# Performance work log

Hardware: AMD Instinct MI355X
Metric: run time of the kernel (lower is better)

Reference implementation:

```python
import jax, jax.numpy as jnp
import numpy as np
import math

NUM_HEADS = 16
D_KV = 64
D_MODEL = 1024
NUM_BUCKETS = 32
MAX_DISTANCE = 128
SEQ = 2048
BATCH = 2


def _relative_position_bucket(relative_position):
    # bidirectional T5 bucketing
    num_buckets = NUM_BUCKETS // 2  # 16
    buckets = (relative_position > 0).astype(jnp.int32) * num_buckets
    rp = jnp.abs(relative_position)
    max_exact = num_buckets // 2  # 8
    is_small = rp < max_exact
    rp_safe = jnp.maximum(rp, 1)  # avoid log(0); masked by is_small anyway
    rp_large = max_exact + (
        jnp.log(rp_safe.astype(jnp.float32) / max_exact)
        / math.log(MAX_DISTANCE / max_exact)
        * (num_buckets - max_exact)
    ).astype(jnp.int32)
    rp_large = jnp.minimum(rp_large, num_buckets - 1)
    return buckets + jnp.where(is_small, rp, rp_large)


def _position_bias(rel_bias_table, q_len, k_len):
    ctx = jnp.arange(q_len)[:, None]
    mem = jnp.arange(k_len)[None, :]
    buckets = _relative_position_bucket(mem - ctx)  # (q,k)
    vals = rel_bias_table[buckets]  # (q,k,h)
    return jnp.transpose(vals, (2, 0, 1))[None]  # (1,h,q,k)


def setup_inputs() -> dict:
    key = jax.random.key(0)
    ks = jax.random.split(key, 6)
    s = 1.0 / math.sqrt(D_MODEL)
    return {
        "hidden_states": jax.random.normal(ks[0], (BATCH, SEQ, D_MODEL), jnp.float32),
        "Wq": jax.random.normal(ks[1], (D_MODEL, NUM_HEADS * D_KV), jnp.float32) * s,
        "Wk": jax.random.normal(ks[2], (D_MODEL, NUM_HEADS * D_KV), jnp.float32) * s,
        "Wv": jax.random.normal(ks[3], (D_MODEL, NUM_HEADS * D_KV), jnp.float32) * s,
        "Wo": jax.random.normal(ks[4], (NUM_HEADS * D_KV, D_MODEL), jnp.float32) * s,
        "rel_bias_table": jax.random.normal(ks[5], (NUM_BUCKETS, NUM_HEADS), jnp.float32),
    }


def reference(hidden_states, Wq, Wk, Wv, Wo, rel_bias_table):
    b, s, _ = hidden_states.shape
    q = (hidden_states @ Wq).reshape(b, s, NUM_HEADS, D_KV).transpose(0, 2, 1, 3)
    k = (hidden_states @ Wk).reshape(b, s, NUM_HEADS, D_KV).transpose(0, 2, 1, 3)
    v = (hidden_states @ Wv).reshape(b, s, NUM_HEADS, D_KV).transpose(0, 2, 1, 3)
    # T5: NO query scaling, additive relative-position bias
    scores = jnp.einsum("bhqd,bhkd->bhqk", q, k) + _position_bias(rel_bias_table, s, s)
    attn = jax.nn.softmax(scores, axis=-1)  # dropout is identity in eval
    out = jnp.einsum("bhqk,bhkd->bhqd", attn, v)
    out = out.transpose(0, 2, 1, 3).reshape(b, s, NUM_HEADS * D_KV)
    return out @ Wo
```

## Files before the change

### kernel.cpp

```cpp
#include <hip/hip_runtime.h>
#include <hip/hip_bf16.h>
#include <math.h>

#define NUM_HEADS 16
#define D_KV 64
#define D_MODEL 1024
#define SEQ 2048
#define BATCH 2
#define LOG2E 1.4426950408889634f

using bf16x8 = __attribute__((ext_vector_type(8))) short;
using bf16x4 = __attribute__((ext_vector_type(4))) short;
using f32x4  = __attribute__((ext_vector_type(4))) float;

__device__ inline unsigned short f2bf(float f) {
  union { float f; unsigned int i; } v; v.f = f;
  unsigned int u = v.i;
  return (unsigned short)((u + 0x7FFFu + ((u >> 16) & 1u)) >> 16);
}
__device__ inline unsigned short f2bf_fast(float f) {
  union { float f; unsigned int i; } v; v.f = f;
  return (unsigned short)((v.i + 0x8000u) >> 16);
}

#if __has_builtin(__builtin_amdgcn_exp2f)
#define EXP2(x) __builtin_amdgcn_exp2f(x)
#else
#define EXP2(x) __expf((x) * 0.6931471805599453f)
#endif

__device__ inline unsigned int pk_bf16(float a, float b) {
#if __has_builtin(__builtin_amdgcn_cvt_pk_bf16_f32)
  auto v = __builtin_amdgcn_cvt_pk_bf16_f32(a, b);
  unsigned int u; __builtin_memcpy(&u, &v, 4);
  return u;
#else
  return ((unsigned int)f2bf_fast(b) << 16) | f2bf_fast(a);
#endif
}

__device__ inline void gld_lds16(const unsigned short* g, unsigned short* l) {
  __builtin_amdgcn_global_load_lds(
      (const __attribute__((address_space(1))) unsigned int*)g,
      (__attribute__((address_space(3))) unsigned int*)l, 16, 0, 0);
}

__global__ __launch_bounds__(256) void prep_kernel(const float* __restrict__ X,
                                                   const float* __restrict__ W0,
                                                   const float* __restrict__ W1,
                                                   const float* __restrict__ W2,
                                                   const float* __restrict__ W3,
                                                   const float* __restrict__ tbl,
                                                   unsigned short* __restrict__ xbf,
                                                   unsigned short* __restrict__ wt,
                                                   float* __restrict__ biasF) {
  __shared__ __align__(16) unsigned short T[64][72];
  int bid = blockIdx.x;
  int t = threadIdx.x;
  if (bid < 2048) {
    int i = (bid * 256 + t) * 8;
    __align__(16) unsigned short tmp[8];
#pragma unroll
    for (int e = 0; e < 8; e++) tmp[e] = f2bf(X[i + e]);
    *(uint4*)&xbf[i] = *(uint4*)tmp;
  } else if (bid < 3072) {
    int rem = bid - 2048;
    int z = rem >> 8, tid = rem & 255;
    const float* in = (z == 0) ? W0 : (z == 1) ? W1 : (z == 2) ? W2 : W3;
    unsigned short* o = wt + (long)z * 1048576;
    int r0 = (tid & 15) * 64, c0 = (tid >> 4) * 64;
#pragma unroll
    for (int i = 0; i < 2; i++) {
      int c = t + 256 * i; int r = c >> 3, k8 = (c & 7) * 8;
      const float* src = &in[(long)(r0 + r) * 1024 + c0 + k8];
      __align__(16) unsigned short tmp[8];
#pragma unroll
      for (int e = 0; e < 8; e++) tmp[e] = f2bf(src[e]);
      *(uint4*)&T[r][k8] = *(uint4*)tmp;
    }
    __syncthreads();
#pragma unroll
    for (int i = 0; i < 2; i++) {
      int c = t + 256 * i; int r = c >> 3, k8 = (c & 7) * 8;
      __align__(16) unsigned short tmp[8];
#pragma unroll
      for (int e = 0; e < 8; e++) tmp[e] = T[k8 + e][r];
      *(uint4*)&o[(long)(c0 + r) * 1024 + r0 + k8] = *(uint4*)tmp;
    }
  } else {
#pragma unroll
    for (int ii = 0; ii < 16; ii++) {
      int idx = t + 256 * ii;
      if (idx >= 4095) break;
      int rel = idx - 2047;
      int bucket = (rel > 0) ? 16 : 0;
      int rp = rel < 0 ? -rel : rel;
      int add;
      if (rp < 8) add = rp;
      else {
        int rl = 8 + (int)(logf((float)rp * 0.125f) / logf(16.0f) * 8.0f);
        add = rl < 15 ? rl : 15;
      }
      bucket += add;
#pragma unroll
      for (int h = 0; h < 16; h++) biasF[h * 4096 + idx] = tbl[bucket * 16 + h] * LOG2E;
    }
  }
}

__global__ __launch_bounds__(256) void gemm_kernel(const unsigned short* __restrict__ X,
                                                   const unsigned short* __restrict__ Wt,
                                                   unsigned short* __restrict__ out_b,
                                                   unsigned short* __restrict__ out_vt,
                                                   float* __restrict__ out_f, int mode) {
  __shared__ __align__(16) unsigned short SMEM[128 * 136];
  unsigned short* As = SMEM;
  unsigned short* Bs = SMEM + 128 * 32;
  const int K = 1024;
  int m0 = blockIdx.x * 128;
  int n0 = blockIdx.y * 128;
  const unsigned short* W = Wt + (long)blockIdx.z * 1048576;
  unsigned short* outq = (mode == 0) ? out_b + (long)blockIdx.z * 4194304 : nullptr;
  float scale = (mode == 0 && blockIdx.z == 0) ? LOG2E : 1.0f;
  int t = threadIdx.x;
  int w = t >> 6, l = t & 63;
  int wr = (w >> 1) * 64, wc = (w & 1) * 64;
  int lr = l & 15, lq = l >> 4;
  f32x4 acc[4][4];
#pragma unroll
  for (int i = 0; i < 4; i++)
#pragma unroll
    for (int j = 0; j < 4; j++) acc[i][j] = (f32x4){0.f, 0.f, 0.f, 0.f};

  for (int k0 = 0; k0 < K; k0 += 32) {
#pragma unroll
    for (int i = 0; i < 2; i++) {
      int c = t + 256 * i;
      int r = c >> 2, kc = (c & 3) * 8;
      gld_lds16(&X[(long)(m0 + r) * K + k0 + kc], &As[c * 8]);
      gld_lds16(&W[(long)(n0 + r) * K + k0 + kc], &Bs[c * 8]);
    }
    __syncthreads();
    bf16x8 a[4], b[4];
#pragma unroll
    for (int mi = 0; mi < 4; mi++) a[mi] = *(const bf16x8*)&As[(wr + mi * 16 + lr) * 32 + lq * 8];
#pragma unroll
    for (int ni = 0; ni < 4; ni++) b[ni] = *(const bf16x8*)&Bs[(wc + ni * 16 + lr) * 32 + lq * 8];
#pragma unroll
    for (int mi = 0; mi < 4; mi++)
#pragma unroll
      for (int ni = 0; ni < 4; ni++)
        acc[mi][ni] = __builtin_amdgcn_mfma_f32_16x16x32_bf16(a[mi], b[ni], acc[mi][ni], 0, 0, 0);
    __syncthreads();
  }

  if (mode == 1) {
    float* Csf = (float*)SMEM;
#pragma unroll
    for (int p = 0; p < 2; p++) {
      if ((w >> 1) == p) {
#pragma unroll
        for (int mi = 0; mi < 4; mi++)
#pragma unroll
          for (int ni = 0; ni < 4; ni++)
#pragma unroll
            for (int r = 0; r < 4; r++)
              Csf[(mi * 16 + lq * 4 + r) * 132 + wc + ni * 16 + lr] = acc[mi][ni][r];
      }
      __syncthreads();
#pragma unroll
      for (int i = 0; i < 8; i++) {
        int c = t + 256 * i;
        int row = c >> 5, ch = c & 31;
        float4 v = *(const float4*)&Csf[row * 132 + ch * 4];
        *(float4*)&out_f[(long)(m0 + p * 64 + row) * 1024 + n0 + ch * 4] = v;
      }
      __syncthreads();
    }
  } else if (blockIdx.z == 2) {
    unsigned short* Cs = SMEM;
#pragma unroll
    for (int mi = 0; mi < 4; mi++)
#pragma unroll
      for (int ni = 0; ni < 4; ni++) {
        int nl = wc + ni * 16 + lr;
        int ml = wr + mi * 16 + lq * 4;
        unsigned int s0 = ((unsigned int)f2bf(acc[mi][ni][1]) << 16) | f2bf(acc[mi][ni][0]);
        unsigned int s1 = ((unsigned int)f2bf(acc[mi][ni][3]) << 16) | f2bf(acc[mi][ni][2]);
        *(uint2*)&Cs[nl * 136 + ml] = (uint2){s0, s1};
      }
    __syncthreads();
    int b2 = m0 >> 11, sbase = m0 & 2047;
#pragma unroll
    for (int i = 0; i < 8; i++) {
      int c = t + 256 * i;
      int row = c >> 4, ch = c & 15;
      uint4 v = *(const uint4*)&Cs[row * 136 + ch * 8];
      int n = n0 + row, h = n >> 6, d = n & 63;
      *(uint4*)&out_vt[(((long)(b2 * 16 + h) * 64 + d) << 11) + sbase + ch * 8] = v;
    }
  } else {
    unsigned short* Cs = SMEM;
#pragma unroll
    for (int mi = 0; mi < 4; mi++)
#pragma unroll
      for (int ni = 0; ni < 4; ni++)
#pragma unroll
        for (int r = 0; r < 4; r++)
          Cs[(wr + mi * 16 + lq * 4 + r) * 136 + wc + ni * 16 + lr] = f2bf(acc[mi][ni][r] * scale);
    __syncthreads();
    int b2 = m0 >> 11, sbase = m0 & 2047;
#pragma unroll
    for (int i = 0; i < 8; i++) {
      int c = t + 256 * i;
      int row = c >> 4, ch = c & 15;
      uint4 v = *(const uint4*)&Cs[row * 136 + ch * 8];
      int n = n0 + ch * 8, h = n >> 6, d = n & 63;
      *(uint4*)&outq[((long)(b2 * 16 + h) * 2048 + sbase + row) * 64 + d] = v;
    }
  }
}

__global__ __launch_bounds__(512) void attn_kernel(const unsigned short* __restrict__ Q,
                                                   const unsigned short* __restrict__ Km,
                                                   const unsigned short* __restrict__ Vt,
                                                   const float* __restrict__ biasF,
                                                   unsigned short* __restrict__ O) {
  __shared__ __align__(16) unsigned short KV[4][4608];
  __shared__ float biasS[2176];
  int q0 = blockIdx.x * 128;
  int bh = blockIdx.y;
  int b_ = bh >> 4, h = bh & 15;
  const unsigned short* Qb = Q  + (long)bh * SEQ * 64;
  const unsigned short* Kb = Km + (long)bh * SEQ * 64;
  const unsigned short* Vb = Vt + (long)bh * 64 * SEQ;
  const float* btabF = biasF + h * 4096;
  int t = threadIdx.x;
  int w = t >> 6, l = t & 63;
  int g = w >> 2, wg = w & 3;
  int lr = l & 15, lq = l >> 4;
  int qw = wg * 32;

  int gbase = 1920 - q0;
  for (int i = t; i < 2176; i += 512) {
    int gi = gbase + i; if (gi > 4094) gi = 4094;
    biasS[i] = btabF[gi];
  }

  bf16x8 aq[2][2];
#pragma unroll
  for (int qt = 0; qt < 2; qt++)
#pragma unroll
    for (int ks = 0; ks < 2; ks++)
      aq[qt][ks] = *(const bf16x8*)&Qb[(long)(q0 + qw + qt * 16 + lr) * 64 + ks * 32 + lq * 8];

  int rs = t >> 3, fs = (t & 7) * 8;

  uint4 kpa = *(const uint4*)&Kb[(long)rs * 64 + fs];
  uint4 kpb = *(const uint4*)&Kb[(long)(64 + rs) * 64 + fs];
  uint4 vpa = *(const uint4*)&Vb[(long)rs * SEQ + fs];
  uint4 vpb = *(const uint4*)&Vb[(long)rs * SEQ + 64 + fs];
  *(uint4*)&KV[0][rs * 72 + fs] = kpa;
  *(uint4*)&KV[1][rs * 72 + fs] = kpb;
  *(uint4*)&KV[2][rs * 72 + fs] = vpa;
  *(uint4*)&KV[3][rs * 72 + fs] = vpb;

  f32x4 accO[4][2];
  f32x4 accL[2];
#pragma unroll
  for (int qt = 0; qt < 2; qt++) {
    accL[qt] = (f32x4){0.f, 0.f, 0.f, 0.f};
#pragma unroll
    for (int dt = 0; dt < 4; dt++) accO[dt][qt] = (f32x4){0.f, 0.f, 0.f, 0.f};
  }

  bf16x4 ones4;
#pragma unroll
  for (int e = 0; e < 4; e++) ones4[e] = (short)0x3F80;

  int vb = 127 + lq * 4 - qw - lr;
  int pbc = vb - 16;

  for (int i = 0; i < 16; i++) {
    __syncthreads();
    int k0 = (2 * i + g) * 64;
    bool more = i < 15;

    float bbl[5][4];
    int pb = pbc + k0;
#pragma unroll
    for (int m = 0; m < 5; m++)
#pragma unroll
      for (int j = 0; j < 4; j++) bbl[m][j] = biasS[pb + 16 * m + j];

    bf16x8 bk[4][2];
#pragma unroll
    for (int kt = 0; kt < 4; kt++)
#pragma unroll
      for (int ks = 0; ks < 2; ks++)
        bk[kt][ks] = *(const bf16x8*)&KV[g][(kt * 16 + lr) * 72 + ks * 32 + lq * 8];

    if (more) {
      const unsigned short* Kn = Kb + (long)(2 * i + 2) * 64 * 64;
      const unsigned short* Vn = Vb + (2 * i + 2) * 64;
      kpa = *(const uint4*)&Kn[(long)rs * 64 + fs];
      kpb = *(const uint4*)&Kn[(long)(64 + rs) * 64 + fs];
      vpa = *(const uint4*)&Vn[(long)rs * SEQ + fs];
      vpb = *(const uint4*)&Vn[(long)rs * SEQ + 64 + fs];
    }

    f32x4 sacc[4][2];
#pragma unroll
    for (int kt = 0; kt < 4; kt++)
#pragma unroll
      for (int qt = 0; qt < 2; qt++) sacc[kt][qt] = (f32x4){0.f, 0.f, 0.f, 0.f};
#pragma unroll
    for (int ks = 0; ks < 2; ks++)
#pragma unroll
      for (int kt = 0; kt < 4; kt++)
#pragma unroll
        for (int qt = 0; qt < 2; qt++)
          sacc[kt][qt] = __builtin_amdgcn_mfma_f32_16x16x32_bf16(bk[kt][ks], aq[qt][ks], sacc[kt][qt], 0, 0, 0);

    bf16x4 pk[4][2];
#pragma unroll
    for (int kt = 0; kt < 4; kt++)
#pragma unroll
      for (int qt = 0; qt < 2; qt++) {
        int blk = kt - qt + 1;
        float p0 = EXP2(sacc[kt][qt][0] + bbl[blk][0]);
        float p1 = EXP2(sacc[kt][qt][1] + bbl[blk][1]);
        float p2 = EXP2(sacc[kt][qt][2] + bbl[blk][2]);
        float p3 = EXP2(sacc[kt][qt][3] + bbl[blk][3]);
        unsigned int uu[2] = { pk_bf16(p0, p1), pk_bf16(p2, p3) };
        bf16x4 pv; __builtin_memcpy(&pv, uu, 8);
        pk[kt][qt] = pv;
      }

#pragma unroll
    for (int kt = 0; kt < 4; kt++) {
      bf16x4 va[4];
#pragma unroll
      for (int dt = 0; dt < 4; dt++)
        va[dt] = *(const bf16x4*)&KV[2 + g][(dt * 16 + lr) * 72 + kt * 16 + lq * 4];
#pragma unroll
      for (int qt = 0; qt < 2; qt++) {
#pragma unroll
        for (int dt = 0; dt < 4; dt++)
          accO[dt][qt] = __builtin_amdgcn_mfma_f32_16x16x16bf16_1k(va[dt], pk[kt][qt], accO[dt][qt], 0, 0, 0);
        accL[qt] = __builtin_amdgcn_mfma_f32_16x16x16bf16_1k(ones4, pk[kt][qt], accL[qt], 0, 0, 0);
      }
    }

    __syncthreads();
    if (more) {
      *(uint4*)&KV[0][rs * 72 + fs] = kpa;
      *(uint4*)&KV[1][rs * 72 + fs] = kpb;
      *(uint4*)&KV[2][rs * 72 + fs] = vpa;
      *(uint4*)&KV[3][rs * 72 + fs] = vpb;
    }
  }

  float* mrg = (float*)&KV[0][0];
  int slot = (wg * 64 + l) * 34;
  if (g == 1) {
    float2* mp = (float2*)&mrg[slot];
    int j = 0;
#pragma unroll
    for (int dt = 0; dt < 4; dt++)
#pragma unroll
      for (int qt = 0; qt < 2; qt++) {
        mp[j++] = (float2){accO[dt][qt][0], accO[dt][qt][1]};
        mp[j++] = (float2){accO[dt][qt][2], accO[dt][qt][3]};
      }
    mp[16] = (float2){accL[0][0], accL[1][0]};
  }
  __syncthreads();
  if (g == 0) {
    const float2* mp = (const float2*)&mrg[slot];
    int j = 0;
#pragma unroll
    for (int dt = 0; dt < 4; dt++)
#pragma unroll
      for (int qt = 0; qt < 2; qt++) {
        float2 a = mp[j++], b2 = mp[j++];
        accO[dt][qt][0] += a.x;  accO[dt][qt][1] += a.y;
        accO[dt][qt][2] += b2.x; accO[dt][qt][3] += b2.y;
      }
    float2 ls = mp[16];
    float rl0 = 1.0f / (accL[0][0] + ls.x);
    float rl1 = 1.0f / (accL[1][0] + ls.y);
#pragma unroll
    for (int qt = 0; qt < 2; qt++) {
      float rl = qt ? rl1 : rl0;
      int q = q0 + qw + qt * 16 + lr;
#pragma unroll
      for (int dt = 0; dt < 4; dt++) {
        unsigned int s0 = ((unsigned int)f2bf(accO[dt][qt][1] * rl) << 16) | f2bf(accO[dt][qt][0] * rl);
        unsigned int s1 = ((unsigned int)f2bf(accO[dt][qt][3] * rl) << 16) | f2bf(accO[dt][qt][2] * rl);
        *(uint2*)&O[((long)(b_ * SEQ + q)) * 1024 + h * 64 + dt * 16 + lq * 4] = (uint2){s0, s1};
      }
    }
  }
}

extern "C" void kernel_launch(void* const* d_in, const int* in_sizes, int n_in,
                              void* d_out, int out_size, void* d_ws, size_t ws_size,
                              hipStream_t stream) {
  const float* X   = (const float*)d_in[0];
  const float* Wq  = (const float*)d_in[1];
  const float* Wk  = (const float*)d_in[2];
  const float* Wv  = (const float*)d_in[3];
  const float* Wo  = (const float*)d_in[4];
  const float* tbl = (const float*)d_in[5];

  unsigned short* wt    = (unsigned short*)d_ws;
  unsigned short* xbf   = wt + 4 * 1048576;
  unsigned short* q_ws  = xbf + 4194304;
  unsigned short* k_ws  = q_ws + 4194304;
  unsigned short* v_ws  = k_ws + 4194304;
  unsigned short* vt_ws = v_ws + 4194304;
  unsigned short* o_ws  = vt_ws + 4194304;
  float* biasF = (float*)(o_ws + 4194304);

  prep_kernel<<<3073, 256, 0, stream>>>(X, Wq, Wk, Wv, Wo, tbl, xbf, wt, biasF);
  gemm_kernel<<<dim3(32, 8, 3), 256, 0, stream>>>(xbf, wt, q_ws, vt_ws, nullptr, 0);
  attn_kernel<<<dim3(16, 32), 512, 0, stream>>>(q_ws, k_ws, vt_ws, biasF, o_ws);
  gemm_kernel<<<dim3(32, 8, 1), 256, 0, stream>>>(o_ws, wt + 3 * 1048576, nullptr, nullptr, (float*)d_out, 1);
}
```

Baseline: 221.1 us.

## Route P through LDS for wider MFMA, compute row sums in ALU, add smaller-tile output GEMM

The attention PV step now writes bf16 probabilities to a per-wave LDS scratch and reads them back as 8-wide fragments. This allows the 16x16x32 MFMA in place of the 16x16x16 form and removes the extra ones-vector MFMA used for row sums. Row sums are accumulated in registers and reduced with lane shuffles. The bias table is stored twice, offset by one, so bias values can be read with aligned float2 loads. The output projection moves to a dedicated 64x64-tile GEMM with a 64-wide K step, giving more blocks. The workspace is also reused for the O buffer and pk_bf16 is used in the V epilogue, at the cost of extra LDS traffic and LDS size in attention.

```diff
diff --git a/kernel.cpp b/kernel.cpp
--- a/kernel.cpp
+++ b/kernel.cpp
@@ -111,8 +111,7 @@
 __global__ __launch_bounds__(256) void gemm_kernel(const unsigned short* __restrict__ X,
                                                    const unsigned short* __restrict__ Wt,
                                                    unsigned short* __restrict__ out_b,
-                                                   unsigned short* __restrict__ out_vt,
-                                                   float* __restrict__ out_f, int mode) {
+                                                   unsigned short* __restrict__ out_vt) {
   __shared__ __align__(16) unsigned short SMEM[128 * 136];
   unsigned short* As = SMEM;
   unsigned short* Bs = SMEM + 128 * 32;
@@ -120,8 +119,8 @@
   int m0 = blockIdx.x * 128;
   int n0 = blockIdx.y * 128;
   const unsigned short* W = Wt + (long)blockIdx.z * 1048576;
-  unsigned short* outq = (mode == 0) ? out_b + (long)blockIdx.z * 4194304 : nullptr;
-  float scale = (mode == 0 && blockIdx.z == 0) ? LOG2E : 1.0f;
+  unsigned short* outq = out_b + (long)blockIdx.z * 4194304;
+  float scale = (blockIdx.z == 0) ? LOG2E : 1.0f;
   int t = threadIdx.x;
   int w = t >> 6, l = t & 63;
   int wr = (w >> 1) * 64, wc = (w & 1) * 64;
@@ -154,30 +153,7 @@
     __syncthreads();
   }
 
-  if (mode == 1) {
-    float* Csf = (float*)SMEM;
-#pragma unroll
-    for (int p = 0; p < 2; p++) {
-      if ((w >> 1) == p) {
-#pragma unroll
-        for (int mi = 0; mi < 4; mi++)
-#pragma unroll
-          for (int ni = 0; ni < 4; ni++)
-#pragma unroll
-            for (int r = 0; r < 4; r++)
-              Csf[(mi * 16 + lq * 4 + r) * 132 + wc + ni * 16 + lr] = acc[mi][ni][r];
-      }
-      __syncthreads();
-#pragma unroll
-      for (int i = 0; i < 8; i++) {
-        int c = t + 256 * i;
-        int row = c >> 5, ch = c & 31;
-        float4 v = *(const float4*)&Csf[row * 132 + ch * 4];
-        *(float4*)&out_f[(long)(m0 + p * 64 + row) * 1024 + n0 + ch * 4] = v;
-      }
-      __syncthreads();
-    }
-  } else if (blockIdx.z == 2) {
+  if (blockIdx.z == 2) {
     unsigned short* Cs = SMEM;
 #pragma unroll
     for (int mi = 0; mi < 4; mi++)
@@ -185,8 +161,8 @@
       for (int ni = 0; ni < 4; ni++) {
         int nl = wc + ni * 16 + lr;
         int ml = wr + mi * 16 + lq * 4;
-        unsigned int s0 = ((unsigned int)f2bf(acc[mi][ni][1]) << 16) | f2bf(acc[mi][ni][0]);
-        unsigned int s1 = ((unsigned int)f2bf(acc[mi][ni][3]) << 16) | f2bf(acc[mi][ni][2]);
+        unsigned int s0 = pk_bf16(acc[mi][ni][0], acc[mi][ni][1]);
+        unsigned int s1 = pk_bf16(acc[mi][ni][2], acc[mi][ni][3]);
         *(uint2*)&Cs[nl * 136 + ml] = (uint2){s0, s1};
       }
     __syncthreads();
@@ -221,13 +197,78 @@
   }
 }
 
+__global__ __launch_bounds__(256) void ogemm_kernel(const unsigned short* __restrict__ X,
+                                                    const unsigned short* __restrict__ W,
+                                                    float* __restrict__ out) {
+  __shared__ __align__(16) unsigned char SMEM[64 * 68 * 4];
+  unsigned short* As = (unsigned short*)SMEM;
+  unsigned short* Bs = As + 4096;
+  float* Csf = (float*)SMEM;
+  const int K = 1024;
+  int m0 = blockIdx.x * 64;
+  int n0 = blockIdx.y * 64;
+  int t = threadIdx.x;
+  int w = t >> 6, l = t & 63;
+  int wr = (w >> 1) * 32, wc = (w & 1) * 32;
+  int lr = l & 15, lq = l >> 4;
+  f32x4 acc[2][2];
+#pragma unroll
+  for (int i = 0; i < 2; i++)
+#pragma unroll
+    for (int j = 0; j < 2; j++) acc[i][j] = (f32x4){0.f, 0.f, 0.f, 0.f};
+
+  for (int k0 = 0; k0 < K; k0 += 64) {
+#pragma unroll
+    for (int i = 0; i < 2; i++) {
+      int c = t + 256 * i;
+      int p = c >> 8, r = (c >> 2) & 63, kc = (c & 3) * 8;
+      gld_lds16(&X[(long)(m0 + r) * K + k0 + p * 32 + kc], &As[c * 8]);
+      gld_lds16(&W[(long)(n0 + r) * K + k0 + p * 32 + kc], &Bs[c * 8]);
+    }
+    __syncthreads();
+    bf16x8 a[2][2], b[2][2];
+#pragma unroll
+    for (int ks = 0; ks < 2; ks++) {
+#pragma unroll
+      for (int mi = 0; mi < 2; mi++) a[mi][ks] = *(const bf16x8*)&As[ks * 2048 + (wr + mi * 16 + lr) * 32 + lq * 8];
+#pragma unroll
+      for (int ni = 0; ni < 2; ni++) b[ni][ks] = *(const bf16x8*)&Bs[ks * 2048 + (wc + ni * 16 + lr) * 32 + lq * 8];
+    }
+#pragma unroll
+    for (int ks = 0; ks < 2; ks++)
+#pragma unroll
+      for (int mi = 0; mi < 2; mi++)
+#pragma unroll
+        for (int ni = 0; ni < 2; ni++)
+          acc[mi][ni] = __builtin_amdgcn_mfma_f32_16x16x32_bf16(a[mi][ks], b[ni][ks], acc[mi][ni], 0, 0, 0);
+    __syncthreads();
+  }
+
+#pragma unroll
+  for (int mi = 0; mi < 2; mi++)
+#pragma unroll
+    for (int ni = 0; ni < 2; ni++)
+#pragma unroll
+      for (int r = 0; r < 4; r++)
+        Csf[(wr + mi * 16 + lq * 4 + r) * 68 + wc + ni * 16 + lr] = acc[mi][ni][r];
+  __syncthreads();
+#pragma unroll
+  for (int i = 0; i < 4; i++) {
+    int c = t + 256 * i;
+    int row = c >> 4, ch = c & 15;
+    float4 v = *(const float4*)&Csf[row * 68 + ch * 4];
+    *(float4*)&out[(long)(m0 + row) * 1024 + n0 + ch * 4] = v;
+  }
+}
+
 __global__ __launch_bounds__(512) void attn_kernel(const unsigned short* __restrict__ Q,
                                                    const unsigned short* __restrict__ Km,
                                                    const unsigned short* __restrict__ Vt,
                                                    const float* __restrict__ biasF,
                                                    unsigned short* __restrict__ O) {
   __shared__ __align__(16) unsigned short KV[4][4608];
-  __shared__ float biasS[2176];
+  __shared__ __align__(16) float biasRf[2][2176];
+  __shared__ __align__(16) unsigned short Ps[8 * 1280];
   int q0 = blockIdx.x * 128;
   int bh = blockIdx.y;
   int b_ = bh >> 4, h = bh & 15;
@@ -243,8 +284,10 @@
 
   int gbase = 1920 - q0;
   for (int i = t; i < 2176; i += 512) {
-    int gi = gbase + i; if (gi > 4094) gi = 4094;
-    biasS[i] = btabF[gi];
+    int g0 = gbase + i;     if (g0 > 4094) g0 = 4094;
+    int g1 = gbase + i + 1; if (g1 > 4094) g1 = 4094;
+    biasRf[0][i] = btabF[g0];
+    biasRf[1][i] = btabF[g1];
   }
 
   bf16x8 aq[2][2];
@@ -266,32 +309,30 @@
   *(uint4*)&KV[3][rs * 72 + fs] = vpb;
 
   f32x4 accO[4][2];
-  f32x4 accL[2];
-#pragma unroll
-  for (int qt = 0; qt < 2; qt++) {
-    accL[qt] = (f32x4){0.f, 0.f, 0.f, 0.f};
+  float rsum[2] = {0.f, 0.f};
+#pragma unroll
+  for (int qt = 0; qt < 2; qt++)
 #pragma unroll
     for (int dt = 0; dt < 4; dt++) accO[dt][qt] = (f32x4){0.f, 0.f, 0.f, 0.f};
-  }
-
-  bf16x4 ones4;
-#pragma unroll
-  for (int e = 0; e < 4; e++) ones4[e] = (short)0x3F80;
 
   int vb = 127 + lq * 4 - qw - lr;
-  int pbc = vb - 16;
+  int bj2 = vb & 1;
+  const float* brow = biasRf[bj2];
+  int pbc = vb - bj2 - 16;
+  unsigned short* Pw = Ps + w * 1280;
 
   for (int i = 0; i < 16; i++) {
     __syncthreads();
     int k0 = (2 * i + g) * 64;
     bool more = i < 15;
 
-    float bbl[5][4];
+    float2 bbl[5][2];
     int pb = pbc + k0;
 #pragma unroll
-    for (int m = 0; m < 5; m++)
-#pragma unroll
-      for (int j = 0; j < 4; j++) bbl[m][j] = biasS[pb + 16 * m + j];
+    for (int m = 0; m < 5; m++) {
+      bbl[m][0] = *(const float2*)&brow[pb + 16 * m];
+      bbl[m][1] = *(const float2*)&brow[pb + 16 * m + 2];
+    }
 
     bf16x8 bk[4][2];
 #pragma unroll
@@ -322,34 +363,36 @@
         for (int qt = 0; qt < 2; qt++)
           sacc[kt][qt] = __builtin_amdgcn_mfma_f32_16x16x32_bf16(bk[kt][ks], aq[qt][ks], sacc[kt][qt], 0, 0, 0);
 
-    bf16x4 pk[4][2];
-#pragma unroll
-    for (int kt = 0; kt < 4; kt++)
-#pragma unroll
-      for (int qt = 0; qt < 2; qt++) {
-        int blk = kt - qt + 1;
-        float p0 = EXP2(sacc[kt][qt][0] + bbl[blk][0]);
-        float p1 = EXP2(sacc[kt][qt][1] + bbl[blk][1]);
-        float p2 = EXP2(sacc[kt][qt][2] + bbl[blk][2]);
-        float p3 = EXP2(sacc[kt][qt][3] + bbl[blk][3]);
-        unsigned int uu[2] = { pk_bf16(p0, p1), pk_bf16(p2, p3) };
-        bf16x4 pv; __builtin_memcpy(&pv, uu, 8);
-        pk[kt][qt] = pv;
-      }
-
-#pragma unroll
-    for (int kt = 0; kt < 4; kt++) {
-      bf16x4 va[4];
+#pragma unroll
+    for (int ktp = 0; ktp < 2; ktp++) {
+#pragma unroll
+      for (int kth = 0; kth < 2; kth++) {
+        int kt = ktp * 2 + kth;
+#pragma unroll
+        for (int qt = 0; qt < 2; qt++) {
+          int blk = kt - qt + 1;
+          float p0 = EXP2(sacc[kt][qt][0] + bbl[blk][0].x);
+          float p1 = EXP2(sacc[kt][qt][1] + bbl[blk][0].y);
+          float p2 = EXP2(sacc[kt][qt][2] + bbl[blk][1].x);
+          float p3 = EXP2(sacc[kt][qt][3] + bbl[blk][1].y);
+          rsum[qt] += (p0 + p1) + (p2 + p3);
+          *(uint2*)&Pw[(qt * 16 + lr) * 40 + kth * 16 + lq * 4] =
+              (uint2){ pk_bf16(p0, p1), pk_bf16(p2, p3) };
+        }
+      }
+      bf16x8 va8[4];
 #pragma unroll
       for (int dt = 0; dt < 4; dt++)
-        va[dt] = *(const bf16x4*)&KV[2 + g][(dt * 16 + lr) * 72 + kt * 16 + lq * 4];
-#pragma unroll
-      for (int qt = 0; qt < 2; qt++) {
+        va8[dt] = *(const bf16x8*)&KV[2 + g][(dt * 16 + lr) * 72 + ktp * 32 + lq * 8];
+      bf16x8 pb8[2];
+#pragma unroll
+      for (int qt = 0; qt < 2; qt++)
+        pb8[qt] = *(const bf16x8*)&Pw[(qt * 16 + lr) * 40 + lq * 8];
+#pragma unroll
+      for (int qt = 0; qt < 2; qt++)
 #pragma unroll
         for (int dt = 0; dt < 4; dt++)
-          accO[dt][qt] = __builtin_amdgcn_mfma_f32_16x16x16bf16_1k(va[dt], pk[kt][qt], accO[dt][qt], 0, 0, 0);
-        accL[qt] = __builtin_amdgcn_mfma_f32_16x16x16bf16_1k(ones4, pk[kt][qt], accL[qt], 0, 0, 0);
-      }
+          accO[dt][qt] = __builtin_amdgcn_mfma_f32_16x16x32_bf16(va8[dt], pb8[qt], accO[dt][qt], 0, 0, 0);
     }
 
     __syncthreads();
@@ -361,6 +404,12 @@
     }
   }
 
+#pragma unroll
+  for (int qt = 0; qt < 2; qt++) {
+    rsum[qt] += __shfl_xor(rsum[qt], 16);
+    rsum[qt] += __shfl_xor(rsum[qt], 32);
+  }
+
   float* mrg = (float*)&KV[0][0];
   int slot = (wg * 64 + l) * 34;
   if (g == 1) {
@@ -373,7 +422,7 @@
         mp[j++] = (float2){accO[dt][qt][0], accO[dt][qt][1]};
         mp[j++] = (float2){accO[dt][qt][2], accO[dt][qt][3]};
       }
-    mp[16] = (float2){accL[0][0], accL[1][0]};
+    mp[16] = (float2){rsum[0], rsum[1]};
   }
   __syncthreads();
   if (g == 0) {
@@ -388,8 +437,8 @@
         accO[dt][qt][2] += b2.x; accO[dt][qt][3] += b2.y;
       }
     float2 ls = mp[16];
-    float rl0 = 1.0f / (accL[0][0] + ls.x);
-    float rl1 = 1.0f / (accL[1][0] + ls.y);
+    float rl0 = 1.0f / (rsum[0] + ls.x);
+    float rl1 = 1.0f / (rsum[1] + ls.y);
 #pragma unroll
     for (int qt = 0; qt < 2; qt++) {
       float rl = qt ? rl1 : rl0;
@@ -418,13 +467,12 @@
   unsigned short* xbf   = wt + 4 * 1048576;
   unsigned short* q_ws  = xbf + 4194304;
   unsigned short* k_ws  = q_ws + 4194304;
-  unsigned short* v_ws  = k_ws + 4194304;
-  unsigned short* vt_ws = v_ws + 4194304;
-  unsigned short* o_ws  = vt_ws + 4194304;
-  float* biasF = (float*)(o_ws + 4194304);
+  unsigned short* vt_ws = k_ws + 4194304;
+  float* biasF = (float*)(vt_ws + 4194304);
+  unsigned short* o_ws  = xbf;
 
   prep_kernel<<<3073, 256, 0, stream>>>(X, Wq, Wk, Wv, Wo, tbl, xbf, wt, biasF);
-  gemm_kernel<<<dim3(32, 8, 3), 256, 0, stream>>>(xbf, wt, q_ws, vt_ws, nullptr, 0);
+  gemm_kernel<<<dim3(32, 8, 3), 256, 0, stream>>>(xbf, wt, q_ws, vt_ws);
   attn_kernel<<<dim3(16, 32), 512, 0, stream>>>(q_ws, k_ws, vt_ws, biasF, o_ws);
-  gemm_kernel<<<dim3(32, 8, 1), 256, 0, stream>>>(o_ws, wt + 3 * 1048576, nullptr, nullptr, (float*)d_out, 1);
-}
+  ogemm_kernel<<<dim3(64, 16), 256, 0, stream>>>(o_ws, wt + 3 * 1048576, (float*)d_out);
+}
```

Result: faster. 212.4 us (-3.9%).
